# Optimization experiments

Measured on AMD Instinct MI355X. Metric: run time of the kernel, lower is better.

The kernel has to match this reference:

```python
import jax, jax.numpy as jnp
import numpy as np

B, Q, K, H, DV = 16, 256, 256, 256, 256


def setup_inputs() -> dict:
    key = jax.random.key(0)
    ks = jax.random.split(key, 6)
    return {
        "queries": jax.random.normal(ks[0], (B, Q, H), dtype=jnp.float32),
        "keys": jax.random.normal(ks[1], (B, K, H), dtype=jnp.float32),
        "values": jax.random.normal(ks[2], (B, K, DV), dtype=jnp.float32),
        "W_q": jax.random.normal(ks[3], (H, H), dtype=jnp.float32) / np.sqrt(H),
        "W_k": jax.random.normal(ks[4], (H, H), dtype=jnp.float32) / np.sqrt(H),
        "w_v": jax.random.normal(ks[5], (H,), dtype=jnp.float32) / np.sqrt(H),
    }


def reference(queries, keys, values, W_q, W_k, w_v):
    # Linear projections (nn.Linear: x @ W.T), bias-free
    q = jnp.einsum("bqd,hd->bqh", queries, W_q)  # [B,Q,H]
    k = jnp.einsum("bkd,hd->bkh", keys, W_k)      # [B,K,H]
    # Broadcast add -> tanh -> scalar projection
    features = jnp.tanh(q[:, :, None, :] + k[:, None, :, :])  # [B,Q,K,H]
    scores = jnp.einsum("bqkh,h->bqk", features, w_v)          # [B,Q,K]
    attn = jax.nn.softmax(scores, axis=-1)                      # [B,Q,K]
    return jnp.einsum("bqk,bkv->bqv", attn, values)            # [B,Q,DV]
```

## Files before the change

kernel.cpp:

```cpp
#include <hip/hip_runtime.h>

#define Bn 16
#define Qn 256
#define Kn 256
#define Hn 256
#define DVn 256

constexpr float C2    = 2.8853900817779268f;
constexpr float LOG2E = 1.4426950408889634f;

__device__ __forceinline__ float fast_exp2(float x) { return __builtin_amdgcn_exp2f(x); }
__device__ __forceinline__ float fast_rcp(float x)  { return __builtin_amdgcn_rcpf(x); }

__global__ __launch_bounds__(256)
void proj_exp_kernel(const float* __restrict__ A, const float* __restrict__ Bm,
                     float* __restrict__ C, int N)
{
    const int m0 = blockIdx.y * 64;
    const int n0 = blockIdx.x * 64;
    __shared__ __align__(16) float As[16][68];
    __shared__ __align__(16) float Bs[16][68];
    const int tid = threadIdx.x;
    const int tx = tid & 15, ty = tid >> 4;
    const int lr = tid >> 2, lk4 = (tid & 3) * 4;
    float acc[4][4] = {};
    for (int k0 = 0; k0 < Hn; k0 += 16) {
        float4 a = *(const float4*)(A  + (size_t)(m0 + lr) * Hn + k0 + lk4);
        float4 w = *(const float4*)(Bm + (size_t)(n0 + lr) * Hn + k0 + lk4);
        As[lk4+0][lr] = a.x; As[lk4+1][lr] = a.y; As[lk4+2][lr] = a.z; As[lk4+3][lr] = a.w;
        Bs[lk4+0][lr] = w.x; Bs[lk4+1][lr] = w.y; Bs[lk4+2][lr] = w.z; Bs[lk4+3][lr] = w.w;
        __syncthreads();
        #pragma unroll
        for (int kk = 0; kk < 16; ++kk) {
            float4 av = *(const float4*)&As[kk][ty*4];
            float4 bv = *(const float4*)&Bs[kk][tx*4];
            const float ar[4] = {av.x, av.y, av.z, av.w};
            const float br[4] = {bv.x, bv.y, bv.z, bv.w};
            #pragma unroll
            for (int i = 0; i < 4; ++i)
                #pragma unroll
                for (int j = 0; j < 4; ++j)
                    acc[i][j] = fmaf(ar[i], br[j], acc[i][j]);
        }
        __syncthreads();
    }
    #pragma unroll
    for (int i = 0; i < 4; ++i) {
        float4 o;
        o.x = fast_exp2(C2 * acc[i][0]);
        o.y = fast_exp2(C2 * acc[i][1]);
        o.z = fast_exp2(C2 * acc[i][2]);
        o.w = fast_exp2(C2 * acc[i][3]);
        *(float4*)(C + (size_t)(m0 + ty*4 + i) * N + n0 + tx*4) = o;
    }
}

__global__ __launch_bounds__(256)
void fused_attn_kernel(const float* __restrict__ Eq, const float* __restrict__ EkT,
                       const float* __restrict__ wv, const float* __restrict__ V,
                       float* __restrict__ out)
{
    const int b  = blockIdx.y;
    const int q0 = blockIdx.x * 4;
    __shared__ __align__(16) float sEq[4 * 256];
    __shared__ __align__(16) float swv[256];
    __shared__ __align__(16) float sP[4 * 260];
    __shared__ float sredM[4][4];
    __shared__ float sredS[4][4];
    const int tid = threadIdx.x;
    {
        const int q = tid >> 6, h4 = (tid & 63) * 4;
        float4 v = *(const float4*)(Eq + (size_t)(b*Qn + q0 + q) * Hn + h4);
        *(float4*)&sEq[q*256 + h4] = v;
        swv[tid] = wv[tid];
    }
    __syncthreads();

    float sc[4] = {0.f, 0.f, 0.f, 0.f};
    const float* ekp = EkT + (size_t)b * Kn + tid;
    for (int h0 = 0; h0 < Hn; h0 += 8) {
        float ek[8];
        #pragma unroll
        for (int j = 0; j < 8; ++j) ek[j] = ekp[(size_t)(h0 + j) * (Bn * Kn)];
        const float4 wa = *(const float4*)&swv[h0];
        const float4 wb = *(const float4*)&swv[h0 + 4];
        #pragma unroll
        for (int q = 0; q < 4; ++q) {
            const float4 ea = *(const float4*)&sEq[q*256 + h0];
            const float4 eb = *(const float4*)&sEq[q*256 + h0 + 4];
            float a = sc[q];
            a = fmaf(wa.x, fast_rcp(fmaf(ea.x, ek[0], 1.f)), a);
            a = fmaf(wa.y, fast_rcp(fmaf(ea.y, ek[1], 1.f)), a);
            a = fmaf(wa.z, fast_rcp(fmaf(ea.z, ek[2], 1.f)), a);
            a = fmaf(wa.w, fast_rcp(fmaf(ea.w, ek[3], 1.f)), a);
            a = fmaf(wb.x, fast_rcp(fmaf(eb.x, ek[4], 1.f)), a);
            a = fmaf(wb.y, fast_rcp(fmaf(eb.y, ek[5], 1.f)), a);
            a = fmaf(wb.z, fast_rcp(fmaf(eb.z, ek[6], 1.f)), a);
            a = fmaf(wb.w, fast_rcp(fmaf(eb.w, ek[7], 1.f)), a);
            sc[q] = a;
        }
    }

    const int w = tid >> 6, lane = tid & 63;
    #pragma unroll
    for (int q = 0; q < 4; ++q) {
        sc[q] = -2.0f * sc[q];
        float mx = sc[q];
        #pragma unroll
        for (int off = 32; off; off >>= 1) mx = fmaxf(mx, __shfl_xor(mx, off, 64));
        if (lane == 0) sredM[q][w] = mx;
    }
    __syncthreads();
    float p[4];
    #pragma unroll
    for (int q = 0; q < 4; ++q) {
        const float mx = fmaxf(fmaxf(sredM[q][0], sredM[q][1]),
                               fmaxf(sredM[q][2], sredM[q][3]));
        p[q] = fast_exp2(LOG2E * (sc[q] - mx));
        float s = p[q];
        #pragma unroll
        for (int off = 32; off; off >>= 1) s += __shfl_xor(s, off, 64);
        if (lane == 0) sredS[q][w] = s;
        sP[q*260 + tid] = p[q];
    }
    __syncthreads();
    float rinv[4];
    #pragma unroll
    for (int q = 0; q < 4; ++q)
        rinv[q] = fast_rcp(sredS[q][0] + sredS[q][1] + sredS[q][2] + sredS[q][3]);

    float acc[4] = {0.f, 0.f, 0.f, 0.f};
    const float* Vb = V + (size_t)b * Kn * DVn + tid;
    for (int k = 0; k < Kn; k += 4) {
        float vv[4];
        #pragma unroll
        for (int j = 0; j < 4; ++j) vv[j] = Vb[(size_t)(k + j) * DVn];
        #pragma unroll
        for (int q = 0; q < 4; ++q) {
            const float4 pq = *(const float4*)&sP[q*260 + k];
            float a = acc[q];
            a = fmaf(pq.x, vv[0], a);
            a = fmaf(pq.y, vv[1], a);
            a = fmaf(pq.z, vv[2], a);
            a = fmaf(pq.w, vv[3], a);
            acc[q] = a;
        }
    }
    float* ob = out + (size_t)(b*Qn + q0) * DVn + tid;
    #pragma unroll
    for (int q = 0; q < 4; ++q)
        ob[(size_t)q * DVn] = acc[q] * rinv[q];
}

extern "C" void kernel_launch(void* const* d_in, const int* in_sizes, int n_in,
                              void* d_out, int out_size, void* d_ws, size_t ws_size,
                              hipStream_t stream) {
    const float* queries = (const float*)d_in[0];
    const float* keys    = (const float*)d_in[1];
    const float* values  = (const float*)d_in[2];
    const float* W_q     = (const float*)d_in[3];
    const float* W_k     = (const float*)d_in[4];
    const float* w_v     = (const float*)d_in[5];
    float* out = (float*)d_out;

    float* Eq  = (float*)d_ws;
    float* EkT = Eq + (size_t)Bn * Qn * Hn;

    proj_exp_kernel<<<dim3(4, 64), 256, 0, stream>>>(queries, W_q, Eq, 256);
    proj_exp_kernel<<<dim3(64, 4), 256, 0, stream>>>(W_k, keys, EkT, 4096);
    fused_attn_kernel<<<dim3(64, 16), 256, 0, stream>>>(Eq, EkT, w_v, values, out);
}
```

Baseline: 149.7 us.

## Merge projection launches, double-buffer GEMM tiles, store Ek in float4-interleaved layout

The two projection GEMMs become one launch, with blockIdx.z choosing queries or keys. The shared-memory tiles are double-buffered so the next global load overlaps the current compute, which removes one barrier per step. Ek is written in a per-batch layout with groups of 4 h values interleaved per key, so the attention kernel can read it with float4 loads instead of strided scalar loads. This trades a more complex store index for fewer launches and better-coalesced, vectorized reads in the dominant score loop.

```diff
diff --git a/kernel.cpp b/kernel.cpp
--- a/kernel.cpp
+++ b/kernel.cpp
@@ -13,27 +13,42 @@
 __device__ __forceinline__ float fast_rcp(float x)  { return __builtin_amdgcn_rcpf(x); }
 
 __global__ __launch_bounds__(256)
-void proj_exp_kernel(const float* __restrict__ A, const float* __restrict__ Bm,
-                     float* __restrict__ C, int N)
+void proj_exp_kernel(const float* __restrict__ q, const float* __restrict__ kx,
+                     const float* __restrict__ wq, const float* __restrict__ wk,
+                     float* __restrict__ Eq, float* __restrict__ Ek)
 {
+    const int z = blockIdx.z;
+    const float* A = z ? kx : q;
+    const float* W = z ? wk : wq;
     const int m0 = blockIdx.y * 64;
     const int n0 = blockIdx.x * 64;
-    __shared__ __align__(16) float As[16][68];
-    __shared__ __align__(16) float Bs[16][68];
+    __shared__ __align__(16) float As[2][16][68];
+    __shared__ __align__(16) float Bs[2][16][68];
     const int tid = threadIdx.x;
     const int tx = tid & 15, ty = tid >> 4;
     const int lr = tid >> 2, lk4 = (tid & 3) * 4;
+    const float* Arow = A + (size_t)(m0 + lr) * Hn + lk4;
+    const float* Wrow = W + (size_t)(n0 + lr) * Hn + lk4;
+    {
+        float4 a = *(const float4*)(Arow);
+        float4 w = *(const float4*)(Wrow);
+        As[0][lk4+0][lr] = a.x; As[0][lk4+1][lr] = a.y; As[0][lk4+2][lr] = a.z; As[0][lk4+3][lr] = a.w;
+        Bs[0][lk4+0][lr] = w.x; Bs[0][lk4+1][lr] = w.y; Bs[0][lk4+2][lr] = w.z; Bs[0][lk4+3][lr] = w.w;
+    }
+    __syncthreads();
     float acc[4][4] = {};
+    int cur = 0;
     for (int k0 = 0; k0 < Hn; k0 += 16) {
-        float4 a = *(const float4*)(A  + (size_t)(m0 + lr) * Hn + k0 + lk4);
-        float4 w = *(const float4*)(Bm + (size_t)(n0 + lr) * Hn + k0 + lk4);
-        As[lk4+0][lr] = a.x; As[lk4+1][lr] = a.y; As[lk4+2][lr] = a.z; As[lk4+3][lr] = a.w;
-        Bs[lk4+0][lr] = w.x; Bs[lk4+1][lr] = w.y; Bs[lk4+2][lr] = w.z; Bs[lk4+3][lr] = w.w;
-        __syncthreads();
+        float4 an, wn;
+        const bool more = (k0 + 16 < Hn);
+        if (more) {
+            an = *(const float4*)(Arow + k0 + 16);
+            wn = *(const float4*)(Wrow + k0 + 16);
+        }
         #pragma unroll
         for (int kk = 0; kk < 16; ++kk) {
-            float4 av = *(const float4*)&As[kk][ty*4];
-            float4 bv = *(const float4*)&Bs[kk][tx*4];
+            float4 av = *(const float4*)&As[cur][kk][ty*4];
+            float4 bv = *(const float4*)&Bs[cur][kk][tx*4];
             const float ar[4] = {av.x, av.y, av.z, av.w};
             const float br[4] = {bv.x, bv.y, bv.z, bv.w};
             #pragma unroll
@@ -42,7 +57,13 @@
                 for (int j = 0; j < 4; ++j)
                     acc[i][j] = fmaf(ar[i], br[j], acc[i][j]);
         }
-        __syncthreads();
+        if (more) {
+            const int nxt = cur ^ 1;
+            As[nxt][lk4+0][lr] = an.x; As[nxt][lk4+1][lr] = an.y; As[nxt][lk4+2][lr] = an.z; As[nxt][lk4+3][lr] = an.w;
+            Bs[nxt][lk4+0][lr] = wn.x; Bs[nxt][lk4+1][lr] = wn.y; Bs[nxt][lk4+2][lr] = wn.z; Bs[nxt][lk4+3][lr] = wn.w;
+            __syncthreads();
+            cur = nxt;
+        }
     }
     #pragma unroll
     for (int i = 0; i < 4; ++i) {
@@ -51,12 +72,19 @@
         o.y = fast_exp2(C2 * acc[i][1]);
         o.z = fast_exp2(C2 * acc[i][2]);
         o.w = fast_exp2(C2 * acc[i][3]);
-        *(float4*)(C + (size_t)(m0 + ty*4 + i) * N + n0 + tx*4) = o;
+        if (z == 0) {
+            *(float4*)(Eq + (size_t)(m0 + ty*4 + i) * Hn + n0 + tx*4) = o;
+        } else {
+            const int m  = m0 + ty*4 + i;
+            const int bq = m >> 8, kk2 = m & 255;
+            const int h  = n0 + tx*4;
+            *(float4*)(Ek + (size_t)bq * (Kn*Hn) + (size_t)(h >> 2) * (Kn*4) + kk2*4) = o;
+        }
     }
 }
 
 __global__ __launch_bounds__(256)
-void fused_attn_kernel(const float* __restrict__ Eq, const float* __restrict__ EkT,
+void fused_attn_kernel(const float* __restrict__ Eq, const float* __restrict__ Ek,
                        const float* __restrict__ wv, const float* __restrict__ V,
                        float* __restrict__ out)
 {
@@ -77,11 +105,11 @@
     __syncthreads();
 
     float sc[4] = {0.f, 0.f, 0.f, 0.f};
-    const float* ekp = EkT + (size_t)b * Kn + tid;
-    for (int h0 = 0; h0 < Hn; h0 += 8) {
-        float ek[8];
-        #pragma unroll
-        for (int j = 0; j < 8; ++j) ek[j] = ekp[(size_t)(h0 + j) * (Bn * Kn)];
+    const float* ekp = Ek + (size_t)b * (Kn*Hn) + (size_t)tid * 4;
+    for (int hg = 0; hg < 64; hg += 2) {
+        const float4 e0 = *(const float4*)(ekp + hg * (Kn*4));
+        const float4 e1 = *(const float4*)(ekp + hg * (Kn*4) + (Kn*4));
+        const int h0 = hg * 4;
         const float4 wa = *(const float4*)&swv[h0];
         const float4 wb = *(const float4*)&swv[h0 + 4];
         #pragma unroll
@@ -89,14 +117,14 @@
             const float4 ea = *(const float4*)&sEq[q*256 + h0];
             const float4 eb = *(const float4*)&sEq[q*256 + h0 + 4];
             float a = sc[q];
-            a = fmaf(wa.x, fast_rcp(fmaf(ea.x, ek[0], 1.f)), a);
-            a = fmaf(wa.y, fast_rcp(fmaf(ea.y, ek[1], 1.f)), a);
-            a = fmaf(wa.z, fast_rcp(fmaf(ea.z, ek[2], 1.f)), a);
-            a = fmaf(wa.w, fast_rcp(fmaf(ea.w, ek[3], 1.f)), a);
-            a = fmaf(wb.x, fast_rcp(fmaf(eb.x, ek[4], 1.f)), a);
-            a = fmaf(wb.y, fast_rcp(fmaf(eb.y, ek[5], 1.f)), a);
-            a = fmaf(wb.z, fast_rcp(fmaf(eb.z, ek[6], 1.f)), a);
-            a = fmaf(wb.w, fast_rcp(fmaf(eb.w, ek[7], 1.f)), a);
+            a = fmaf(wa.x, fast_rcp(fmaf(ea.x, e0.x, 1.f)), a);
+            a = fmaf(wa.y, fast_rcp(fmaf(ea.y, e0.y, 1.f)), a);
+            a = fmaf(wa.z, fast_rcp(fmaf(ea.z, e0.z, 1.f)), a);
+            a = fmaf(wa.w, fast_rcp(fmaf(ea.w, e0.w, 1.f)), a);
+            a = fmaf(wb.x, fast_rcp(fmaf(eb.x, e1.x, 1.f)), a);
+            a = fmaf(wb.y, fast_rcp(fmaf(eb.y, e1.y, 1.f)), a);
+            a = fmaf(wb.z, fast_rcp(fmaf(eb.z, e1.z, 1.f)), a);
+            a = fmaf(wb.w, fast_rcp(fmaf(eb.w, e1.w, 1.f)), a);
             sc[q] = a;
         }
     }
@@ -163,10 +191,9 @@
     const float* w_v     = (const float*)d_in[5];
     float* out = (float*)d_out;
 
-    float* Eq  = (float*)d_ws;
-    float* EkT = Eq + (size_t)Bn * Qn * Hn;
+    float* Eq = (float*)d_ws;
+    float* Ek = Eq + (size_t)Bn * Qn * Hn;
 
-    proj_exp_kernel<<<dim3(4, 64), 256, 0, stream>>>(queries, W_q, Eq, 256);
-    proj_exp_kernel<<<dim3(64, 4), 256, 0, stream>>>(W_k, keys, EkT, 4096);
-    fused_attn_kernel<<<dim3(64, 16), 256, 0, stream>>>(Eq, EkT, w_v, values, out);
+    proj_exp_kernel<<<dim3(4, 64, 2), 256, 0, stream>>>(queries, keys, W_q, W_k, Eq, Ek);
+    fused_attn_kernel<<<dim3(64, 16), 256, 0, stream>>>(Eq, Ek, w_v, values, out);
 }
```

Result: faster. 133.6 us (-10.8%).
